# Kernel optimization log

Hardware: AMD Instinct MI355X
Metric: run time of the kernel (lower is better)

Reference implementation:

```python
import jax, jax.numpy as jnp
import numpy as np
from jax import lax

N_ITER = 5
SMOOTHNESS_WEIGHT = 1.0
SMOOTHNESS_THETA = 1.0
FILTER_SIZE = 11  # crfseg-style default odd Gaussian filter size


def _gaussian_kernel_1d():
    c = (FILTER_SIZE - 1) / 2.0
    d = jnp.arange(FILTER_SIZE, dtype=jnp.float32) - c
    k = jnp.exp(-(d ** 2) / (2.0 * SMOOTHNESS_THETA ** 2))
    return k / jnp.sum(k)


def _blur(q):
    # q: (B, C, H, W); separable per-channel Gaussian smoothing, 'same' padding
    B, C, H, W = q.shape
    k = _gaussian_kernel_1d()
    r = q.reshape(B * C, 1, H, W)
    dn = ('NCHW', 'OIHW', 'NCHW')
    r = lax.conv_general_dilated(r, k.reshape(1, 1, FILTER_SIZE, 1), (1, 1), 'SAME', dimension_numbers=dn)
    r = lax.conv_general_dilated(r, k.reshape(1, 1, 1, FILTER_SIZE), (1, 1), 'SAME', dimension_numbers=dn)
    return r.reshape(B, C, H, W)


def setup_inputs() -> dict:
    key = jax.random.key(0)
    k1, k2 = jax.random.split(key)
    x = jax.random.normal(k1, (16, 3, 512, 512), dtype=jnp.float32)
    conv_w = jax.random.normal(k2, (2, 3, 3, 3), dtype=jnp.float32) * 0.1
    conv_b = jnp.zeros((2,), dtype=jnp.float32)
    return {"x": x, "conv_w": conv_w, "conv_b": conv_b}


def reference(x, conv_w, conv_b):
    # backbone: simple 3x3 conv producing per-class logits (B, C, H, W)
    dn = ('NCHW', 'OIHW', 'NCHW')
    logits = lax.conv_general_dilated(x, conv_w, (1, 1), 'SAME', dimension_numbers=dn)
    logits = logits + conv_b[None, :, None, None]

    # mean-field CRF: compatibility mu(k,k') = -(k==k') => message = -blur(q)
    unary = logits
    cur = logits
    for _ in range(N_ITER):
        q = jax.nn.softmax(cur, axis=1)
        cur = unary + SMOOTHNESS_WEIGHT * _blur(q)
    return cur
```

## Files before the change

kernel.cpp:

```cpp
#include <hip/hip_runtime.h>

constexpr int BB = 16;
constexpr int HH = 512;
constexpr int WW = 512;
constexpr int HW = HH * WW;
constexpr int NP1 = BB * HW;

using half_t = _Float16;
using half2v = __attribute__((ext_vector_type(2))) _Float16;
using half8v = __attribute__((ext_vector_type(8))) _Float16;

__device__ constexpr float GK[11] = {
    1.4867195147342977e-06f,
    1.3383022576488537e-04f,
    4.4318484119380075e-03f,
    5.3990966513188063e-02f,
    2.4197072451914337e-01f,
    3.9894228040143270e-01f,
    2.4197072451914337e-01f,
    5.3990966513188063e-02f,
    4.4318484119380075e-03f,
    1.3383022576488537e-04f,
    1.4867195147342977e-06f,
};
__device__ constexpr float PFX[6] = {
    0.0f,
    1.4867195147342977e-06f,
    1.3531694527962e-04f,
    4.5671653572176e-03f,
    5.8558131870406e-02f,
    3.0052885638955e-01f,
};

__device__ __forceinline__ float edgeS(int i) {
    float s = 1.f;
    if (i < 5)   s -= PFX[5 - i];
    if (i > 506) s -= PFX[i - 506];
    return s;
}

__device__ __forceinline__ float sig1(float d) {
    d = fminf(fmaxf(d, -30.f), 30.f);
    float e = __expf(d);
    return e * __builtin_amdgcn_rcpf(1.f + e);
}

__global__ __launch_bounds__(256) void conv3x3_du(
    const float* __restrict__ x, const float* __restrict__ w,
    const float* __restrict__ bias, half_t* __restrict__ u0p,
    half_t* __restrict__ dup)
{
    int bid = blockIdx.x;
    int sb  = (bid & 7) * 128 + (bid >> 3);
    int t   = sb * 256 + threadIdx.x;
    int b   = t >> 14;
    int rem = t & 16383;
    int y0  = (rem >> 6) << 1;
    int xs  = (rem & 63) << 3;

    float W[54];
#pragma unroll
    for (int i = 0; i < 13; ++i)
        *(float4*)&W[4 * i] = *(const float4*)(w + 4 * i);
    W[52] = w[52];
    W[53] = w[53];
    float b0 = bias[0], b1 = bias[1];

    float acc0[2][8], acc1[2][8];
#pragma unroll
    for (int r = 0; r < 2; ++r)
#pragma unroll
        for (int j = 0; j < 8; ++j) { acc0[r][j] = b0; acc1[r][j] = b1; }

    const float* xb = x + (size_t)b * 3 * HW;
#pragma unroll
    for (int ci = 0; ci < 3; ++ci) {
        const float* xc = xb + ci * HW;
#pragma unroll
        for (int iy = 0; iy < 4; ++iy) {
            int yy = y0 - 1 + iy;
            if (yy < 0 || yy >= HH) continue;
            const float* r = xc + yy * WW;
            float4 cA = *(const float4*)(r + xs);
            float4 cB = *(const float4*)(r + xs + 4);
            float l  = (xs > 0)      ? r[xs - 1] : 0.f;
            float rr = (xs < WW - 8) ? r[xs + 8] : 0.f;
            float v[10] = {l, cA.x, cA.y, cA.z, cA.w,
                           cB.x, cB.y, cB.z, cB.w, rr};
#pragma unroll
            for (int orow = 0; orow < 2; ++orow) {
                int kh = iy - orow;
                if (kh < 0 || kh > 2) continue;
                float w00 = W[ci * 9 + kh * 3 + 0];
                float w01 = W[ci * 9 + kh * 3 + 1];
                float w02 = W[ci * 9 + kh * 3 + 2];
                float w10 = W[27 + ci * 9 + kh * 3 + 0];
                float w11 = W[27 + ci * 9 + kh * 3 + 1];
                float w12 = W[27 + ci * 9 + kh * 3 + 2];
#pragma unroll
                for (int j = 0; j < 8; ++j) {
                    acc0[orow][j] = fmaf(w00, v[j],
                                    fmaf(w01, v[j + 1],
                                    fmaf(w02, v[j + 2], acc0[orow][j])));
                    acc1[orow][j] = fmaf(w10, v[j],
                                    fmaf(w11, v[j + 1],
                                    fmaf(w12, v[j + 2], acc1[orow][j])));
                }
            }
        }
    }
#pragma unroll
    for (int orow = 0; orow < 2; ++orow) {
        size_t o = (size_t)b * HW + (size_t)(y0 + orow) * WW + xs;
        half8v h0, h1;
#pragma unroll
        for (int j = 0; j < 8; ++j) {
            h0[j] = (half_t)acc0[orow][j];
            h1[j] = (half_t)(acc1[orow][j] - acc0[orow][j]);
        }
        *(half8v*)(u0p + o) = h0;
        *(half8v*)(dup + o) = h1;
    }
}

template <int MODE>
__global__ __launch_bounds__(256) void crf_diff2(
    const half_t* __restrict__ dcur, const half_t* __restrict__ dup,
    const half_t* __restrict__ u0p, half_t* __restrict__ dnxt,
    float* __restrict__ outp)
{
    __shared__ float v[8][528];

    int bid  = blockIdx.x;
    int tile = (bid & 7) * 128 + (bid >> 3);
    int b    = tile >> 6;
    int y0   = (tile & 63) << 3;
    int tid  = threadIdx.x;
    int x0   = tid << 1;

    if (tid < 5) {
#pragma unroll
        for (int r = 0; r < 8; ++r) {
            v[r][tid] = 0.f;
            v[r][517 + tid] = 0.f;
        }
    }

    size_t pb = (size_t)b * HW + x0;

    float acc[8][2] = {{0.f}};
    float raw[8][2];
#pragma unroll
    for (int i = 0; i < 18; ++i) {
        int yy = y0 + i - 5;
        if (yy < 0 || yy >= HH) continue;
        half2v dv = *(const half2v*)(dcur + pb + (size_t)yy * WW);
        float da = (float)dv[0], db_ = (float)dv[1];
        if (MODE == 0) {
            if (i >= 5 && i <= 12) { raw[i - 5][0] = da; raw[i - 5][1] = db_; }
        }
        float qa = sig1(da), qb = sig1(db_);
#pragma unroll
        for (int r = 0; r < 8; ++r) {
            int dt = i - r;
            if (dt < 0 || dt > 10) continue;
            float k = GK[dt];
            acc[r][0] = fmaf(k, qa, acc[r][0]);
            acc[r][1] = fmaf(k, qb, acc[r][1]);
        }
    }
#pragma unroll
    for (int r = 0; r < 8; ++r)
        *(float2*)(&v[r][5 + x0]) = make_float2(acc[r][0], acc[r][1]);
    __syncthreads();

    float SxA = edgeS(x0), SxB = edgeS(x0 + 1);

#pragma unroll
    for (int r = 0; r < 8; ++r) {
        int yy = y0 + r;
        float Sy = edgeS(yy);

        float wv[12];
#pragma unroll
        for (int t = 0; t < 6; ++t)
            *(float2*)&wv[2 * t] = *(const float2*)(&v[r][x0 + 2 * t]);

        float m0 = 0.f, m1 = 0.f;
#pragma unroll
        for (int t = 0; t < 11; ++t) {
            m0 = fmaf(GK[t], wv[t], m0);
            m1 = fmaf(GK[t], wv[t + 1], m1);
        }

        size_t po = pb + (size_t)yy * WW;
        float dua, dub;
        if (MODE == 0) { dua = raw[r][0]; dub = raw[r][1]; }
        else {
            half2v duv = *(const half2v*)(dup + po);
            dua = (float)duv[0]; dub = (float)duv[1];
        }

        float S0 = SxA * Sy, S1 = SxB * Sy;
        if (MODE == 2) {
            half2v u0v = *(const half2v*)(u0p + po);
            float ua = (float)u0v[0], ub = (float)u0v[1];
            size_t oo = (size_t)b * 2 * HW + (size_t)yy * WW + x0;
            *(float2*)(outp + oo)      = make_float2(ua + (S0 - m0),
                                                     ub + (S1 - m1));
            *(float2*)(outp + oo + HW) = make_float2((ua + dua) + m0,
                                                     (ub + dub) + m1);
        } else {
            half2v hw;
            hw[0] = (half_t)(dua + fmaf(2.f, m0, -S0));
            hw[1] = (half_t)(dub + fmaf(2.f, m1, -S1));
            *(half2v*)(dnxt + po) = hw;
        }
    }
}

extern "C" void kernel_launch(void* const* d_in, const int* in_sizes, int n_in,
                              void* d_out, int out_size, void* d_ws, size_t ws_size,
                              hipStream_t stream) {
    const float* x    = (const float*)d_in[0];
    const float* w    = (const float*)d_in[1];
    const float* bias = (const float*)d_in[2];

    float*  out = (float*)d_out;
    half_t* u0p = (half_t*)d_ws;
    half_t* dup = u0p + NP1;
    half_t* dA  = dup + NP1;
    half_t* dB  = dA + NP1;

    conv3x3_du<<<1024, 256, 0, stream>>>(x, w, bias, u0p, dup);
    crf_diff2<0><<<1024, 256, 0, stream>>>(dup, dup, u0p, dA, out);
    crf_diff2<1><<<1024, 256, 0, stream>>>(dA,  dup, u0p, dB, out);
    crf_diff2<1><<<1024, 256, 0, stream>>>(dB,  dup, u0p, dA, out);
    crf_diff2<1><<<1024, 256, 0, stream>>>(dA,  dup, u0p, dB, out);
    crf_diff2<2><<<1024, 256, 0, stream>>>(dB,  dup, u0p, dA, out);
}
```

Measured before the change: 78.43 us.

## Fuse pairs of CRF iterations into one kernel with halo recomputation

Replaces the per-iteration CRF kernels with a kernel that performs two mean-field iterations per launch. It computes an expanded 18-row intermediate band in shared memory so the second iteration's vertical halo is available locally. This removes two kernel launches and two global read/write passes of the intermediate fp16 difference maps. In exchange it recomputes halo rows, needs more shared memory, and raises register pressure, which may reduce occupancy.

```diff
diff --git a/kernel.cpp b/kernel.cpp
--- a/kernel.cpp
+++ b/kernel.cpp
@@ -123,13 +123,11 @@
     }
 }
 
-template <int MODE>
-__global__ __launch_bounds__(256) void crf_diff2(
-    const half_t* __restrict__ dcur, const half_t* __restrict__ dup,
-    const half_t* __restrict__ u0p, half_t* __restrict__ dnxt,
-    float* __restrict__ outp)
+__global__ __launch_bounds__(256) void crf_pair(
+    const half_t* __restrict__ sp, const half_t* __restrict__ dup,
+    half_t* __restrict__ dnxt)
 {
-    __shared__ float v[8][528];
+    __shared__ float v[18][528];
 
     int bid  = blockIdx.x;
     int tile = (bid & 7) * 128 + (bid >> 3);
@@ -140,6 +138,116 @@
 
     if (tid < 5) {
 #pragma unroll
+        for (int r = 0; r < 18; ++r) { v[r][tid] = 0.f; v[r][517 + tid] = 0.f; }
+    }
+
+    size_t pb = (size_t)b * HW + x0;
+    float SxA = edgeS(x0), SxB = edgeS(x0 + 1);
+
+    float st[18][2] = {{0.f}};
+#pragma unroll
+    for (int i = 0; i < 28; ++i) {
+        int yy = y0 + i - 10;
+        if (yy < 0 || yy >= HH) continue;
+        half2v dv = *(const half2v*)(sp + pb + (size_t)yy * WW);
+        float qa = sig1((float)dv[0]), qb = sig1((float)dv[1]);
+#pragma unroll
+        for (int r1 = 0; r1 < 18; ++r1) {
+            int dt = i - r1;
+            if (dt < 0 || dt > 10) continue;
+            float k = GK[dt];
+            st[r1][0] = fmaf(k, qa, st[r1][0]);
+            st[r1][1] = fmaf(k, qb, st[r1][1]);
+        }
+    }
+#pragma unroll
+    for (int r1 = 0; r1 < 18; ++r1)
+        *(float2*)(&v[r1][5 + x0]) = make_float2(st[r1][0], st[r1][1]);
+    __syncthreads();
+
+    float duo[8][2];
+#pragma unroll
+    for (int r1 = 0; r1 < 18; ++r1) {
+        int yy = y0 + r1 - 5;
+        if (yy < 0 || yy >= HH) continue;
+        float wv[12];
+#pragma unroll
+        for (int t = 0; t < 6; ++t)
+            *(float2*)&wv[2 * t] = *(const float2*)(&v[r1][x0 + 2 * t]);
+        float m0 = 0.f, m1 = 0.f;
+#pragma unroll
+        for (int t = 0; t < 11; ++t) {
+            m0 = fmaf(GK[t], wv[t], m0);
+            m1 = fmaf(GK[t], wv[t + 1], m1);
+        }
+        half2v duv = *(const half2v*)(dup + pb + (size_t)yy * WW);
+        float dua = (float)duv[0], dub = (float)duv[1];
+        if (r1 >= 5 && r1 < 13) {
+            duo[r1 - 5][0] = dua;
+            duo[r1 - 5][1] = dub;
+        }
+        float Sy = edgeS(yy);
+        st[r1][0] = dua + fmaf(2.f, m0, -(SxA * Sy));
+        st[r1][1] = dub + fmaf(2.f, m1, -(SxB * Sy));
+    }
+
+    float acc[8][2] = {{0.f}};
+#pragma unroll
+    for (int r1 = 0; r1 < 18; ++r1) {
+        int yy = y0 + r1 - 5;
+        if (yy < 0 || yy >= HH) continue;
+        float qa = sig1(st[r1][0]), qb = sig1(st[r1][1]);
+#pragma unroll
+        for (int r = 0; r < 8; ++r) {
+            int dt = r1 - r;
+            if (dt < 0 || dt > 10) continue;
+            float k = GK[dt];
+            acc[r][0] = fmaf(k, qa, acc[r][0]);
+            acc[r][1] = fmaf(k, qb, acc[r][1]);
+        }
+    }
+    __syncthreads();
+#pragma unroll
+    for (int r = 0; r < 8; ++r)
+        *(float2*)(&v[r][5 + x0]) = make_float2(acc[r][0], acc[r][1]);
+    __syncthreads();
+
+#pragma unroll
+    for (int r = 0; r < 8; ++r) {
+        int yy = y0 + r;
+        float Sy = edgeS(yy);
+        float wv[12];
+#pragma unroll
+        for (int t = 0; t < 6; ++t)
+            *(float2*)&wv[2 * t] = *(const float2*)(&v[r][x0 + 2 * t]);
+        float m0 = 0.f, m1 = 0.f;
+#pragma unroll
+        for (int t = 0; t < 11; ++t) {
+            m0 = fmaf(GK[t], wv[t], m0);
+            m1 = fmaf(GK[t], wv[t + 1], m1);
+        }
+        half2v hw;
+        hw[0] = (half_t)(duo[r][0] + fmaf(2.f, m0, -(SxA * Sy)));
+        hw[1] = (half_t)(duo[r][1] + fmaf(2.f, m1, -(SxB * Sy)));
+        *(half2v*)(dnxt + pb + (size_t)yy * WW) = hw;
+    }
+}
+
+__global__ __launch_bounds__(256) void crf_final(
+    const half_t* __restrict__ dcur, const half_t* __restrict__ dup,
+    const half_t* __restrict__ u0p, float* __restrict__ outp)
+{
+    __shared__ float v[8][528];
+
+    int bid  = blockIdx.x;
+    int tile = (bid & 7) * 128 + (bid >> 3);
+    int b    = tile >> 6;
+    int y0   = (tile & 63) << 3;
+    int tid  = threadIdx.x;
+    int x0   = tid << 1;
+
+    if (tid < 5) {
+#pragma unroll
         for (int r = 0; r < 8; ++r) {
             v[r][tid] = 0.f;
             v[r][517 + tid] = 0.f;
@@ -149,17 +257,12 @@
     size_t pb = (size_t)b * HW + x0;
 
     float acc[8][2] = {{0.f}};
-    float raw[8][2];
 #pragma unroll
     for (int i = 0; i < 18; ++i) {
         int yy = y0 + i - 5;
         if (yy < 0 || yy >= HH) continue;
         half2v dv = *(const half2v*)(dcur + pb + (size_t)yy * WW);
-        float da = (float)dv[0], db_ = (float)dv[1];
-        if (MODE == 0) {
-            if (i >= 5 && i <= 12) { raw[i - 5][0] = da; raw[i - 5][1] = db_; }
-        }
-        float qa = sig1(da), qb = sig1(db_);
+        float qa = sig1((float)dv[0]), qb = sig1((float)dv[1]);
 #pragma unroll
         for (int r = 0; r < 8; ++r) {
             int dt = i - r;
@@ -194,28 +297,17 @@
         }
 
         size_t po = pb + (size_t)yy * WW;
-        float dua, dub;
-        if (MODE == 0) { dua = raw[r][0]; dub = raw[r][1]; }
-        else {
-            half2v duv = *(const half2v*)(dup + po);
-            dua = (float)duv[0]; dub = (float)duv[1];
-        }
+        half2v duv = *(const half2v*)(dup + po);
+        half2v u0v = *(const half2v*)(u0p + po);
+        float dua = (float)duv[0], dub = (float)duv[1];
+        float ua  = (float)u0v[0], ub  = (float)u0v[1];
 
         float S0 = SxA * Sy, S1 = SxB * Sy;
-        if (MODE == 2) {
-            half2v u0v = *(const half2v*)(u0p + po);
-            float ua = (float)u0v[0], ub = (float)u0v[1];
-            size_t oo = (size_t)b * 2 * HW + (size_t)yy * WW + x0;
-            *(float2*)(outp + oo)      = make_float2(ua + (S0 - m0),
-                                                     ub + (S1 - m1));
-            *(float2*)(outp + oo + HW) = make_float2((ua + dua) + m0,
-                                                     (ub + dub) + m1);
-        } else {
-            half2v hw;
-            hw[0] = (half_t)(dua + fmaf(2.f, m0, -S0));
-            hw[1] = (half_t)(dub + fmaf(2.f, m1, -S1));
-            *(half2v*)(dnxt + po) = hw;
-        }
+        size_t oo = (size_t)b * 2 * HW + (size_t)yy * WW + x0;
+        *(float2*)(outp + oo)      = make_float2(ua + (S0 - m0),
+                                                 ub + (S1 - m1));
+        *(float2*)(outp + oo + HW) = make_float2((ua + dua) + m0,
+                                                 (ub + dub) + m1);
     }
 }
 
@@ -233,9 +325,7 @@
     half_t* dB  = dA + NP1;
 
     conv3x3_du<<<1024, 256, 0, stream>>>(x, w, bias, u0p, dup);
-    crf_diff2<0><<<1024, 256, 0, stream>>>(dup, dup, u0p, dA, out);
-    crf_diff2<1><<<1024, 256, 0, stream>>>(dA,  dup, u0p, dB, out);
-    crf_diff2<1><<<1024, 256, 0, stream>>>(dB,  dup, u0p, dA, out);
-    crf_diff2<1><<<1024, 256, 0, stream>>>(dA,  dup, u0p, dB, out);
-    crf_diff2<2><<<1024, 256, 0, stream>>>(dB,  dup, u0p, dA, out);
-}
+    crf_pair<<<1024, 256, 0, stream>>>(dup, dup, dA);
+    crf_pair<<<1024, 256, 0, stream>>>(dA,  dup, dB);
+    crf_final<<<1024, 256, 0, stream>>>(dB, dup, u0p, out);
+}
```

After: 89.96 us. 1.15x slower.
